# Kernel tuning notes

Hardware: AMD Instinct MI355X
Metric: run time of the kernel (lower is better)

The kernel has to match this reference:

```python
import jax, jax.numpy as jnp
import numpy as np

N = 300000
H = 700
W_GRID = 700
CIN = 64
COUT = 64
K = 9


def setup_inputs() -> dict:
    rng = np.random.default_rng(0)
    lin = rng.permutation(H * W_GRID)[:N]
    ys = (lin // W_GRID).astype(np.int64)
    xs = (lin % W_GRID).astype(np.int64)
    grid = np.full(H * W_GRID, -1, np.int32)
    grid[lin] = np.arange(N, dtype=np.int32)
    offs = [(dy, dx) for dy in (-1, 0, 1) for dx in (-1, 0, 1)]

    def build(d):
        nbr = np.full((K, N), -1, np.int32)
        for k, (dy, dx) in enumerate(offs):
            ny = ys + dy * d
            nx = xs + dx * d
            valid = (ny >= 0) & (ny < H) & (nx >= 0) & (nx < W_GRID)
            l = np.clip(ny * W_GRID + nx, 0, H * W_GRID - 1)
            nbr[k] = np.where(valid, grid[l], -1)
        return jnp.asarray(nbr)

    nbr_d1 = build(1)
    nbr_d2 = build(2)

    key = jax.random.key(0)
    ks = jax.random.split(key, 16)
    f32 = jnp.float32

    def bn(k, c):
        s = jax.random.uniform(k, (c,), f32, 0.5, 1.5)
        b = jax.random.normal(jax.random.fold_in(k, 1), (c,), f32) * 0.1
        return s, b

    features = jax.random.normal(ks[0], (N, CIN), f32)
    W1 = jax.random.normal(ks[1], (K, CIN, COUT), f32) * 0.05
    W2a = jax.random.normal(ks[2], (CIN, COUT // 2), f32) * 0.05
    W2b = jax.random.normal(ks[3], (K, COUT // 2, COUT), f32) * 0.05
    W3 = jax.random.normal(ks[4], (K, CIN, COUT), f32) * 0.05
    Wf = jax.random.normal(ks[5], (3 * COUT, COUT), f32) * 0.05
    A1_w = jax.random.normal(ks[6], (3 * COUT, COUT // 4), f32) * 0.1
    A1_b = jnp.zeros((COUT // 4,), f32)
    A2_w = jax.random.normal(ks[7], (COUT // 4, 3 * COUT), f32) * 0.1
    A2_b = jnp.zeros((3 * COUT,), f32)
    bn1_s, bn1_b = bn(ks[8], COUT)
    bn2a_s, bn2a_b = bn(ks[9], COUT // 2)
    bn2b_s, bn2b_b = bn(ks[10], COUT)
    bn3_s, bn3_b = bn(ks[11], COUT)
    bnf_s, bnf_b = bn(ks[12], COUT)

    return dict(features=features, W1=W1, bn1_s=bn1_s, bn1_b=bn1_b,
                W2a=W2a, bn2a_s=bn2a_s, bn2a_b=bn2a_b,
                W2b=W2b, bn2b_s=bn2b_s, bn2b_b=bn2b_b,
                W3=W3, bn3_s=bn3_s, bn3_b=bn3_b,
                A1_w=A1_w, A1_b=A1_b, A2_w=A2_w, A2_b=A2_b,
                Wf=Wf, bnf_s=bnf_s, bnf_b=bnf_b,
                nbr_d1=nbr_d1, nbr_d2=nbr_d2)


def _sconv(f, nbr, W):
    # f: [N, Cin], nbr: [K, N] (-1 = no neighbor), W: [K, Cin, Cout]
    mask = (nbr >= 0)[..., None]                      # [K, N, 1]
    g = jnp.where(mask, f[jnp.clip(nbr, 0)], 0.0)     # [K, N, Cin] gather
    return jnp.einsum('knc,kcd->nd', g, W)            # [N, Cout]


def _bnrelu(x, s, b):
    # inference-mode BatchNorm folded into affine scale/shift, then ReLU
    return jax.nn.relu(x * s + b)


def reference(features, W1, bn1_s, bn1_b, W2a, bn2a_s, bn2a_b, W2b, bn2b_s, bn2b_b,
              W3, bn3_s, bn3_b, A1_w, A1_b, A2_w, A2_b, Wf, bnf_s, bnf_b,
              nbr_d1, nbr_d2):
    # path 1: 3x3 sparse conv + BN + ReLU
    feat1 = _bnrelu(_sconv(features, nbr_d1, W1), bn1_s, bn1_b)
    # path 2: 1x1 bottleneck + 3x3 sparse conv
    h = _bnrelu(features @ W2a, bn2a_s, bn2a_b)
    feat2 = _bnrelu(_sconv(h, nbr_d1, W2b), bn2b_s, bn2b_b)
    # path 3: 3x3 dilated (d=2) sparse conv
    feat3 = _bnrelu(_sconv(features, nbr_d2, W3), bn3_s, bn3_b)
    ms = jnp.concatenate([feat1, feat2, feat3], axis=1)   # [N, 3*Cout]
    # SE-style attention from global max pool over active sites
    pooled = jnp.max(ms, axis=0)                          # [3*Cout]
    attn = jax.nn.sigmoid(jax.nn.relu(pooled @ A1_w + A1_b) @ A2_w + A2_b)
    ms = ms * attn
    # 1x1 fusion conv + BN + ReLU
    fused = _bnrelu(ms @ Wf, bnf_s, bnf_b)                # [N, Cout]
    return fused
```

## Files before the change

kernel.cpp:

```cpp
#include <hip/hip_runtime.h>

#define N_PTS 300000
#define NPAD  300032
#define ZROW  N_PTS

typedef _Float16 f16;
typedef _Float16 f16x8 __attribute__((ext_vector_type(8)));
typedef float    f32x4 __attribute__((ext_vector_type(4)));

__device__ __forceinline__ f16 f2h(float x) { return (f16)x; }

union u4f16 { uint4 u; f16x8 h; };

#define HEAD_BLOCKS (NPAD / 256)
#define WP_BLOCKS   361


__global__ __launch_bounds__(256) void k_head(
    const float* __restrict__ feat, const float* __restrict__ W2a,
    const float* __restrict__ s2a, const float* __restrict__ b2a,
    const float* __restrict__ W1, const float* __restrict__ W2b,
    const float* __restrict__ W3,
    f16* __restrict__ featf, f16* __restrict__ hf,
    f16* __restrict__ Wt1, f16* __restrict__ Wt2b, f16* __restrict__ Wt3,
    float* __restrict__ pooled)
{
    __shared__ f16 sWa[2048];

    if (blockIdx.x >= HEAD_BLOCKS) {
        int i = (blockIdx.x - HEAD_BLOCKS) * 256 + threadIdx.x;
        if (i < 36864) {
            int j = i & 7, lane = (i >> 3) & 63, nt = (i >> 9) & 3,
                ks = (i >> 11) & 1, k = i >> 12;
            int d = ks * 32 + (lane >> 4) * 8 + j, c = nt * 16 + (lane & 15);
            Wt1[i] = f2h(W1[(k << 12) + (d << 6) + c]);
        } else if (i < 73728) {
            int ii = i - 36864;
            int j = ii & 7, lane = (ii >> 3) & 63, nt = (ii >> 9) & 3,
                ks = (ii >> 11) & 1, k = ii >> 12;
            int d = ks * 32 + (lane >> 4) * 8 + j, c = nt * 16 + (lane & 15);
            Wt3[ii] = f2h(W3[(k << 12) + (d << 6) + c]);
        } else if (i < 92160) {
            int ii = i - 73728;
            int j = ii & 7, lane = (ii >> 3) & 63, nt = (ii >> 9) & 3, k = ii >> 11;
            int d = (lane >> 4) * 8 + j, c = nt * 16 + (lane & 15);
            Wt2b[ii] = f2h(W2b[k * 2048 + (d << 6) + c]);
        } else if (i < 92352) {
            pooled[i - 92160] = 0.f;
        }
        return;
    }

    {
        int t = threadIdx.x;
        int lane_ = t & 63, nt_ = (t >> 6) & 1, ks_ = (t >> 7) & 1;
        int ln_ = lane_ & 15, q_ = lane_ >> 4;
#pragma unroll
        for (int j = 0; j < 8; j++)
            sWa[((ks_ * 2 + nt_) * 64 + lane_) * 8 + j] =
                f2h(W2a[(ks_ * 32 + q_ * 8 + j) * 32 + nt_ * 16 + ln_]);
    }
    __syncthreads();

    int lane = threadIdx.x & 63, wave = threadIdx.x >> 6;
    int n0 = (blockIdx.x * 4 + wave) * 64;
    int ln = lane & 15, q = lane >> 4;

    f16x8 a[4][2];
#pragma unroll
    for (int mt = 0; mt < 4; mt++) {
        int n = n0 + mt * 16 + ln;
#pragma unroll
        for (int ks = 0; ks < 2; ks++) {
            u4f16 v;
            if (n < N_PTS) {
                const float* p = feat + (long)n * 64 + ks * 32 + q * 8;
                float4 lo = *(const float4*)p;
                float4 hi = *(const float4*)(p + 4);
                v.h[0] = f2h(lo.x); v.h[1] = f2h(lo.y);
                v.h[2] = f2h(lo.z); v.h[3] = f2h(lo.w);
                v.h[4] = f2h(hi.x); v.h[5] = f2h(hi.y);
                v.h[6] = f2h(hi.z); v.h[7] = f2h(hi.w);
            } else {
                v.u = make_uint4(0u, 0u, 0u, 0u);
            }
            a[mt][ks] = v.h;
            *(uint4*)(featf + (long)n * 64 + ks * 32 + q * 8) = v.u;
        }
    }

    f32x4 acc[4][2];
    for (int mt = 0; mt < 4; mt++) for (int nt = 0; nt < 2; nt++)
        acc[mt][nt] = (f32x4){0.f, 0.f, 0.f, 0.f};
#pragma unroll
    for (int ks = 0; ks < 2; ks++)
#pragma unroll
        for (int nt = 0; nt < 2; nt++) {
            f16x8 b = *(const f16x8*)(sWa + ((ks * 2 + nt) * 64 + lane) * 8);
#pragma unroll
            for (int mt = 0; mt < 4; mt++)
                acc[mt][nt] = __builtin_amdgcn_mfma_f32_16x16x32_f16(a[mt][ks], b, acc[mt][nt], 0, 0, 0);
        }

#pragma unroll
    for (int nt = 0; nt < 2; nt++) {
        int ch = nt * 16 + ln;
        float s = s2a[ch], bb = b2a[ch];
#pragma unroll
        for (int mt = 0; mt < 4; mt++)
#pragma unroll
            for (int r = 0; r < 4; r++) {
                int n = n0 + mt * 16 + q * 4 + r;
                float v = (n < N_PTS) ? fmaxf(acc[mt][nt][r] * s + bb, 0.f) : 0.f;
                hf[(long)n * 32 + ch] = f2h(v);
            }
    }
}

template <int CIN>
__device__ __forceinline__ void loadrows(
    uint4 (&dst)[4][CIN / 32], const int (&idx)[4],
    const f16* __restrict__ src, int q)
{
#pragma unroll
    for (int mt = 0; mt < 4; mt++) {
        const f16* p = src + (long)idx[mt] * CIN + q * 8;
#pragma unroll
        for (int ks = 0; ks < CIN / 32; ks++)
            dst[mt][ks] = *(const uint4*)(p + ks * 32);
    }
}

__device__ __forceinline__ void loadidx(
    int (&dst)[4], const int* __restrict__ nbr, int k, int n0, int ln)
{
    const int* nb = nbr + k * N_PTS;
#pragma unroll
    for (int mt = 0; mt < 4; mt++) {
        int nn = n0 + mt * 16 + ln;
        int v = (nn < N_PTS) ? nb[nn] : -1;
        dst[mt] = (v < 0) ? ZROW : v;
    }
}

template <int CIN>
__device__ __forceinline__ void conv_path(
    const f16* __restrict__ src, const f16* WtL,
    const int* __restrict__ nbr,
    int lane, int n0,
    const float* __restrict__ bns, const float* __restrict__ bnb,
    f16* __restrict__ msf, int colBase, float* __restrict__ pooled)
{
    constexpr int KS = CIN / 32;
    int ln = lane & 15, q = lane >> 4;

    f32x4 acc[4][4];
    for (int mt = 0; mt < 4; mt++) for (int nt = 0; nt < 4; nt++)
        acc[mt][nt] = (f32x4){0.f, 0.f, 0.f, 0.f};

    int  idxr[4][4];
    uint4 raw[4][4][KS];

#pragma unroll
    for (int k = 0; k < 4; k++) loadidx(idxr[k], nbr, k, n0, ln);
#pragma unroll
    for (int k = 0; k < 3; k++) loadrows<CIN>(raw[k], idxr[k], src, q);
    __builtin_amdgcn_sched_barrier(0);

#pragma unroll
    for (int k = 0; k < 9; k++) {
        if (k + 3 < 9) loadrows<CIN>(raw[(k + 3) & 3], idxr[(k + 3) & 3], src, q);
        if (k + 4 < 9) loadidx(idxr[k & 3], nbr, k + 4, n0, ln);
        __builtin_amdgcn_sched_barrier(0);
        const f16* Wk = WtL + k * (KS * 4 * 512);
        __builtin_amdgcn_s_setprio(1);
#pragma unroll
        for (int ks = 0; ks < KS; ks++)
#pragma unroll
            for (int nt = 0; nt < 4; nt++) {
                f16x8 b = *(const f16x8*)(Wk + (ks * 4 + nt) * 512 + lane * 8);
#pragma unroll
                for (int mt = 0; mt < 4; mt++) {
                    u4f16 v; v.u = raw[k & 3][mt][ks];
                    acc[mt][nt] = __builtin_amdgcn_mfma_f32_16x16x32_f16(v.h, b, acc[mt][nt], 0, 0, 0);
                }
            }
        __builtin_amdgcn_s_setprio(0);
    }

#pragma unroll
    for (int nt = 0; nt < 4; nt++) {
        int ch = colBase + nt * 16 + ln;
        float s = bns[nt * 16 + ln], bb = bnb[nt * 16 + ln];
        float cmax = 0.f;
#pragma unroll
        for (int mt = 0; mt < 4; mt++)
#pragma unroll
            for (int r = 0; r < 4; r++) {
                int n = n0 + mt * 16 + q * 4 + r;
                float v = fmaxf(acc[mt][nt][r] * s + bb, 0.f);
                msf[(long)n * 192 + ch] = f2h(v);
                if (n < N_PTS) cmax = fmaxf(cmax, v);
            }
        cmax = fmaxf(cmax, __shfl_xor(cmax, 16));
        cmax = fmaxf(cmax, __shfl_xor(cmax, 32));
        if (q == 0) atomicMax((int*)(pooled + ch), __float_as_int(cmax));
    }
}

__global__ __launch_bounds__(512, 2) void k_conv(
    const f16* __restrict__ featf, const f16* __restrict__ hf,
    const f16* __restrict__ Wt1, const f16* __restrict__ Wt2b, const f16* __restrict__ Wt3,
    const int* __restrict__ nbr1, const int* __restrict__ nbr2,
    const float* __restrict__ bn1_s, const float* __restrict__ bn1_b,
    const float* __restrict__ bn2b_s, const float* __restrict__ bn2b_b,
    const float* __restrict__ bn3_s, const float* __restrict__ bn3_b,
    f16* __restrict__ msf, float* __restrict__ pooled)
{
    __shared__ f16 smem[9 * 64 * 64];

    int path = blockIdx.x % 3;
    int g    = blockIdx.x / 3;
    int lane = threadIdx.x & 63, wave = threadIdx.x >> 6;
    int n0 = (g * 8 + wave) * 64;

    const f16* Wsrc = (path == 0) ? Wt1 : (path == 1) ? Wt2b : Wt3;
    int nchunk = (path == 1) ? (9 * 32 * 64 / 8) : (9 * 64 * 64 / 8);
    for (int i = threadIdx.x; i < nchunk; i += 512)
        ((uint4*)smem)[i] = ((const uint4*)Wsrc)[i];
    __syncthreads();

    if (path == 0)
        conv_path<64>(featf, smem, nbr1, lane, n0, bn1_s,  bn1_b,  msf, 0,   pooled);
    else if (path == 1)
        conv_path<32>(hf,    smem, nbr1, lane, n0, bn2b_s, bn2b_b, msf, 64,  pooled);
    else
        conv_path<64>(featf, smem, nbr2, lane, n0, bn3_s,  bn3_b,  msf, 128, pooled);
}

__global__ __launch_bounds__(512, 2) void k_fuse(
    const f16* __restrict__ msf, const float* __restrict__ pooled,
    const float* __restrict__ A1w, const float* __restrict__ A1b,
    const float* __restrict__ A2w, const float* __restrict__ A2b,
    const float* __restrict__ Wf,
    const float* __restrict__ sf, const float* __restrict__ bf_,
    float* __restrict__ out)
{
    __shared__ float sp[192], sa1[16], sattn[192];
    __shared__ f16 sWf[12288];
    int t = threadIdx.x;
    if (t < 192) sp[t] = pooled[t];
    __syncthreads();
    if (t < 16) {
        float a = A1b[t];
        for (int i = 0; i < 192; i++) a += sp[i] * A1w[i * 16 + t];
        sa1[t] = fmaxf(a, 0.f);
    }
    __syncthreads();
    if (t < 192) {
        float a = A2b[t];
        for (int i = 0; i < 16; i++) a += sa1[i] * A2w[i * 192 + t];
        sattn[t] = 1.f / (1.f + expf(-a));
    }
    __syncthreads();
    for (int i = t; i < 12288; i += 512) {
        int j = i & 7, lane = (i >> 3) & 63, nt = (i >> 9) & 3, kt = i >> 11;
        int jrow = kt * 32 + (lane >> 4) * 8 + j, c = nt * 16 + (lane & 15);
        sWf[i] = f2h(Wf[jrow * 64 + c] * sattn[jrow]);
    }
    __syncthreads();

    int lane = threadIdx.x & 63, wave = threadIdx.x >> 6;
    int n0 = blockIdx.x * 256 + wave * 32;
    int ln = lane & 15, q = lane >> 4;

    uint4 araw[6][2];
#pragma unroll
    for (int kt = 0; kt < 6; kt++)
#pragma unroll
        for (int mt = 0; mt < 2; mt++)
            araw[kt][mt] = *(const uint4*)(msf + (long)(n0 + mt * 16 + ln) * 192 + kt * 32 + q * 8);

    f32x4 acc[2][4];
    for (int mt = 0; mt < 2; mt++) for (int nt = 0; nt < 4; nt++)
        acc[mt][nt] = (f32x4){0.f, 0.f, 0.f, 0.f};

#pragma unroll
    for (int kt = 0; kt < 6; kt++)
#pragma unroll
        for (int nt = 0; nt < 4; nt++) {
            f16x8 b = *(const f16x8*)(sWf + ((kt * 4 + nt) * 64 + lane) * 8);
#pragma unroll
            for (int mt = 0; mt < 2; mt++) {
                u4f16 v; v.u = araw[kt][mt];
                acc[mt][nt] = __builtin_amdgcn_mfma_f32_16x16x32_f16(v.h, b, acc[mt][nt], 0, 0, 0);
            }
        }

#pragma unroll
    for (int nt = 0; nt < 4; nt++) {
        int ch = nt * 16 + ln;
        float s = sf[ch], bb = bf_[ch];
#pragma unroll
        for (int mt = 0; mt < 2; mt++)
#pragma unroll
            for (int r = 0; r < 4; r++) {
                int n = n0 + mt * 16 + q * 4 + r;
                if (n < N_PTS)
                    __builtin_nontemporal_store(fmaxf(acc[mt][nt][r] * s + bb, 0.f),
                                                &out[(long)n * 64 + ch]);
            }
    }
}

extern "C" void kernel_launch(void* const* d_in, const int* in_sizes, int n_in,
                              void* d_out, int out_size, void* d_ws, size_t ws_size,
                              hipStream_t stream)
{
    const float* features = (const float*)d_in[0];
    const float* W1     = (const float*)d_in[1];
    const float* bn1_s  = (const float*)d_in[2];
    const float* bn1_b  = (const float*)d_in[3];
    const float* W2a    = (const float*)d_in[4];
    const float* bn2a_s = (const float*)d_in[5];
    const float* bn2a_b = (const float*)d_in[6];
    const float* W2b    = (const float*)d_in[7];
    const float* bn2b_s = (const float*)d_in[8];
    const float* bn2b_b = (const float*)d_in[9];
    const float* W3     = (const float*)d_in[10];
    const float* bn3_s  = (const float*)d_in[11];
    const float* bn3_b  = (const float*)d_in[12];
    const float* A1w    = (const float*)d_in[13];
    const float* A1b    = (const float*)d_in[14];
    const float* A2w    = (const float*)d_in[15];
    const float* A2b    = (const float*)d_in[16];
    const float* Wf     = (const float*)d_in[17];
    const float* bnf_s  = (const float*)d_in[18];
    const float* bnf_b  = (const float*)d_in[19];
    const int*   nbr1   = (const int*)d_in[20];
    const int*   nbr2   = (const int*)d_in[21];

    char* ws = (char*)d_ws;
    size_t off = 0;
    f16* featf = (f16*)(ws + off); off += (size_t)NPAD * 64 * 2;
    f16* hf    = (f16*)(ws + off); off += (size_t)NPAD * 32 * 2;
    f16* msf   = (f16*)(ws + off); off += (size_t)NPAD * 192 * 2;
    f16* Wt1   = (f16*)(ws + off); off += 9 * 64 * 64 * 2;
    f16* Wt3   = (f16*)(ws + off); off += 9 * 64 * 64 * 2;
    f16* Wt2b  = (f16*)(ws + off); off += 9 * 32 * 64 * 2;
    float* pooled = (float*)(ws + off); off += 256 * 4;

    k_head<<<HEAD_BLOCKS + WP_BLOCKS, 256, 0, stream>>>(
        features, W2a, bn2a_s, bn2a_b, W1, W2b, W3,
        featf, hf, Wt1, Wt2b, Wt3, pooled);

    k_conv<<<(NPAD / 64 / 8) * 3, 512, 0, stream>>>(featf, hf, Wt1, Wt2b, Wt3, nbr1, nbr2,
                                           bn1_s, bn1_b, bn2b_s, bn2b_b, bn3_s, bn3_b,
                                           msf, pooled);

    k_fuse<<<NPAD / 256, 512, 0, stream>>>(msf, pooled, A1w, A1b, A2w, A2b, Wf,
                                           bnf_s, bnf_b, (float*)d_out);
}
```

Measured before the change: 407.4 us.

## Process two row tiles per fuse block and prefetch activations before attention prologue

The fusion kernel now launches half as many blocks, each handling two 256-row tiles, so the attention MLP and attention-scaled weight staging into shared memory run once per two tiles. The first tile's activation loads are issued before the prologue so their latency overlaps the attention computation. The cost is more live registers across the prologue and less parallelism per launch, which may reduce occupancy or tail balance.

```diff
diff --git a/kernel.cpp b/kernel.cpp
--- a/kernel.cpp
+++ b/kernel.cpp
@@ -249,6 +249,18 @@
     __shared__ float sp[192], sa1[16], sattn[192];
     __shared__ f16 sWf[12288];
     int t = threadIdx.x;
+    int lane = t & 63, wave = t >> 6;
+    int ln = lane & 15, q = lane >> 4;
+    int n0a = blockIdx.x * 256 + wave * 32;
+    int n0b = n0a + 586 * 256;
+
+    uint4 arawA[6][2];
+#pragma unroll
+    for (int kt = 0; kt < 6; kt++)
+#pragma unroll
+        for (int mt = 0; mt < 2; mt++)
+            arawA[kt][mt] = *(const uint4*)(msf + (long)(n0a + mt * 16 + ln) * 192 + kt * 32 + q * 8);
+
     if (t < 192) sp[t] = pooled[t];
     __syncthreads();
     if (t < 16) {
@@ -264,52 +276,79 @@
     }
     __syncthreads();
     for (int i = t; i < 12288; i += 512) {
-        int j = i & 7, lane = (i >> 3) & 63, nt = (i >> 9) & 3, kt = i >> 11;
-        int jrow = kt * 32 + (lane >> 4) * 8 + j, c = nt * 16 + (lane & 15);
+        int j = i & 7, ll = (i >> 3) & 63, nt = (i >> 9) & 3, kt = i >> 11;
+        int jrow = kt * 32 + (ll >> 4) * 8 + j, c = nt * 16 + (ll & 15);
         sWf[i] = f2h(Wf[jrow * 64 + c] * sattn[jrow]);
     }
     __syncthreads();
 
-    int lane = threadIdx.x & 63, wave = threadIdx.x >> 6;
-    int n0 = blockIdx.x * 256 + wave * 32;
-    int ln = lane & 15, q = lane >> 4;
-
-    uint4 araw[6][2];
-#pragma unroll
-    for (int kt = 0; kt < 6; kt++)
-#pragma unroll
-        for (int mt = 0; mt < 2; mt++)
-            araw[kt][mt] = *(const uint4*)(msf + (long)(n0 + mt * 16 + ln) * 192 + kt * 32 + q * 8);
-
-    f32x4 acc[2][4];
-    for (int mt = 0; mt < 2; mt++) for (int nt = 0; nt < 4; nt++)
-        acc[mt][nt] = (f32x4){0.f, 0.f, 0.f, 0.f};
-
-#pragma unroll
-    for (int kt = 0; kt < 6; kt++)
+    {
+        f32x4 acc[2][4];
+        for (int mt = 0; mt < 2; mt++) for (int nt = 0; nt < 4; nt++)
+            acc[mt][nt] = (f32x4){0.f, 0.f, 0.f, 0.f};
+#pragma unroll
+        for (int kt = 0; kt < 6; kt++)
+#pragma unroll
+            for (int nt = 0; nt < 4; nt++) {
+                f16x8 b = *(const f16x8*)(sWf + ((kt * 4 + nt) * 64 + lane) * 8);
+#pragma unroll
+                for (int mt = 0; mt < 2; mt++) {
+                    u4f16 v; v.u = arawA[kt][mt];
+                    acc[mt][nt] = __builtin_amdgcn_mfma_f32_16x16x32_f16(v.h, b, acc[mt][nt], 0, 0, 0);
+                }
+            }
 #pragma unroll
         for (int nt = 0; nt < 4; nt++) {
-            f16x8 b = *(const f16x8*)(sWf + ((kt * 4 + nt) * 64 + lane) * 8);
-#pragma unroll
-            for (int mt = 0; mt < 2; mt++) {
-                u4f16 v; v.u = araw[kt][mt];
-                acc[mt][nt] = __builtin_amdgcn_mfma_f32_16x16x32_f16(v.h, b, acc[mt][nt], 0, 0, 0);
-            }
+            int ch = nt * 16 + ln;
+            float s = sf[ch], bb = bf_[ch];
+#pragma unroll
+            for (int mt = 0; mt < 2; mt++)
+#pragma unroll
+                for (int r = 0; r < 4; r++) {
+                    int n = n0a + mt * 16 + q * 4 + r;
+                    if (n < N_PTS)
+                        __builtin_nontemporal_store(fmaxf(acc[mt][nt][r] * s + bb, 0.f),
+                                                    &out[(long)n * 64 + ch]);
+                }
         }
-
-#pragma unroll
-    for (int nt = 0; nt < 4; nt++) {
-        int ch = nt * 16 + ln;
-        float s = sf[ch], bb = bf_[ch];
-#pragma unroll
-        for (int mt = 0; mt < 2; mt++)
-#pragma unroll
-            for (int r = 0; r < 4; r++) {
-                int n = n0 + mt * 16 + q * 4 + r;
-                if (n < N_PTS)
-                    __builtin_nontemporal_store(fmaxf(acc[mt][nt][r] * s + bb, 0.f),
-                                                &out[(long)n * 64 + ch]);
-            }
+    }
+
+    if (n0b < NPAD) {
+        uint4 arawB[6][2];
+#pragma unroll
+        for (int kt = 0; kt < 6; kt++)
+#pragma unroll
+            for (int mt = 0; mt < 2; mt++)
+                arawB[kt][mt] = *(const uint4*)(msf + (long)(n0b + mt * 16 + ln) * 192 + kt * 32 + q * 8);
+
+        f32x4 acc[2][4];
+        for (int mt = 0; mt < 2; mt++) for (int nt = 0; nt < 4; nt++)
+            acc[mt][nt] = (f32x4){0.f, 0.f, 0.f, 0.f};
+#pragma unroll
+        for (int kt = 0; kt < 6; kt++)
+#pragma unroll
+            for (int nt = 0; nt < 4; nt++) {
+                f16x8 b = *(const f16x8*)(sWf + ((kt * 4 + nt) * 64 + lane) * 8);
+#pragma unroll
+                for (int mt = 0; mt < 2; mt++) {
+                    u4f16 v; v.u = arawB[kt][mt];
+                    acc[mt][nt] = __builtin_amdgcn_mfma_f32_16x16x32_f16(v.h, b, acc[mt][nt], 0, 0, 0);
+                }
+            }
+#pragma unroll
+        for (int nt = 0; nt < 4; nt++) {
+            int ch = nt * 16 + ln;
+            float s = sf[ch], bb = bf_[ch];
+#pragma unroll
+            for (int mt = 0; mt < 2; mt++)
+#pragma unroll
+                for (int r = 0; r < 4; r++) {
+                    int n = n0b + mt * 16 + q * 4 + r;
+                    if (n < N_PTS)
+                        __builtin_nontemporal_store(fmaxf(acc[mt][nt][r] * s + bb, 0.f),
+                                                    &out[(long)n * 64 + ch]);
+                }
+        }
     }
 }
 
@@ -358,6 +397,6 @@
                                            bn1_s, bn1_b, bn2b_s, bn2b_b, bn3_s, bn3_b,
                                            msf, pooled);
 
-    k_fuse<<<NPAD / 256, 512, 0, stream>>>(msf, pooled, A1w, A1b, A2w, A2b, Wf,
-                                           bnf_s, bnf_b, (float*)d_out);
-}
+    k_fuse<<<586, 512, 0, stream>>>(msf, pooled, A1w, A1b, A2w, A2b, Wf,
+                                    bnf_s, bnf_b, (float*)d_out);
+}
```

After: 424.4 us. 1.04x slower.
